# Optimization experiments

Hardware: AMD Instinct MI355X
Metric: run time of the kernel (lower is better)

## Reference

```python
import jax, jax.numpy as jnp
import numpy as np

HEADS = 8
DIM_HEAD = 64
SCALE = DIM_HEAD ** -0.5


def setup_inputs() -> dict:
    key = jax.random.key(0)
    ks = jax.random.split(key, 6)
    b, n, d = 2, 4096, 1024
    inner = HEADS * DIM_HEAD  # 512
    x = jax.random.normal(ks[0], (b, n, d), dtype=jnp.float32)
    Wq = jax.random.normal(ks[1], (d, inner), dtype=jnp.float32) * (d ** -0.5)
    Wk = jax.random.normal(ks[2], (d, inner), dtype=jnp.float32) * (d ** -0.5)
    Wv = jax.random.normal(ks[3], (d, inner), dtype=jnp.float32) * (d ** -0.5)
    Wout = jax.random.normal(ks[4], (inner, d), dtype=jnp.float32) * (inner ** -0.5)
    bout = jnp.zeros((d,), dtype=jnp.float32)
    return {"x": x, "Wq": Wq, "Wk": Wk, "Wv": Wv, "Wout": Wout, "bout": bout}


def reference(x, Wq, Wk, Wv, Wout, bout):
    b, n, _ = x.shape
    h, dh = HEADS, DIM_HEAD
    # self-attention: context = x
    q = (x @ Wq).reshape(b, n, h, dh).transpose(0, 2, 1, 3)  # b h n d
    k = (x @ Wk).reshape(b, n, h, dh).transpose(0, 2, 1, 3)
    v = (x @ Wv).reshape(b, n, h, dh).transpose(0, 2, 1, 3)
    sim = jnp.einsum('bhid,bhjd->bhij', q, k) * SCALE  # full score matrix
    attn = jax.nn.softmax(sim, axis=-1)
    out = jnp.einsum('bhij,bhjd->bhid', attn, v)
    out = out.transpose(0, 2, 1, 3).reshape(b, n, h * dh)  # b n (h d)
    return out @ Wout + bout
```

## Files before the change

### kernel.cpp

```cpp
#include <hip/hip_runtime.h>
#include <hip/hip_bf16.h>

typedef __bf16 bf16x8 __attribute__((ext_vector_type(8)));
typedef __bf16 bf16x4 __attribute__((ext_vector_type(4)));
typedef float floatx4 __attribute__((ext_vector_type(4)));

#define MFMA16(a, b, c) __builtin_amdgcn_mfma_f32_16x16x32_bf16((a), (b), (c), 0, 0, 0)

__device__ __forceinline__ void stage16(const __bf16* g, __bf16* lds_base) {
  __builtin_amdgcn_global_load_lds(
      (__attribute__((address_space(1))) void*)(void*)g,
      (__attribute__((address_space(3))) void*)lds_base, 16, 0, 0);
}

__global__ void detect_dtype(const unsigned int* __restrict__ x, int* __restrict__ flag) {
  __shared__ int cnt;
  if (threadIdx.x == 0) cnt = 0;
  __syncthreads();
  int c = 0;
  for (int i = threadIdx.x; i < 4096; i += 256) {
    const unsigned f = (x[i] >> 7) & 0xFF;
    c += (f >= 100 && f <= 140) ? 1 : 0;
  }
  atomicAdd(&cnt, c);
  __syncthreads();
  if (threadIdx.x == 0) *flag = (cnt > 2048) ? 1 : 0;
}

__global__ __launch_bounds__(256) void transpose3_conv(
    const void* __restrict__ s0, const void* __restrict__ s1,
    const void* __restrict__ s2, __bf16* __restrict__ dst,
    int R, int C, const int* __restrict__ flagp) {
  __shared__ __bf16 t[32][33];
  const int isbf = *flagp;
  const void* src = (blockIdx.z == 0) ? s0 : (blockIdx.z == 1) ? s1 : s2;
  __bf16* d = dst + (size_t)blockIdx.z * R * C;
  const int bx = blockIdx.x * 32, by = blockIdx.y * 32;
  const int x = threadIdx.x & 31, y0 = threadIdx.x >> 5;
#pragma unroll
  for (int i = y0; i < 32; i += 8) {
    const size_t idx = (size_t)(by + i) * C + bx + x;
    t[i][x] = isbf ? ((const __bf16*)src)[idx] : (__bf16)(((const float*)src)[idx]);
  }
  __syncthreads();
#pragma unroll
  for (int i = y0; i < 32; i += 8) d[(size_t)(bx + i) * R + by + x] = t[x][i];
}

__global__ __launch_bounds__(256) void transpose_conv(const void* __restrict__ src,
                                                      __bf16* __restrict__ dst,
                                                      int R, int C,
                                                      const int* __restrict__ flagp) {
  __shared__ __bf16 t[32][33];
  const int isbf = *flagp;
  const int bx = blockIdx.x * 32, by = blockIdx.y * 32;
  const int x = threadIdx.x & 31, y0 = threadIdx.x >> 5;
#pragma unroll
  for (int i = y0; i < 32; i += 8) {
    const size_t idx = (size_t)(by + i) * C + bx + x;
    t[i][x] = isbf ? ((const __bf16*)src)[idx] : (__bf16)(((const float*)src)[idx]);
  }
  __syncthreads();
#pragma unroll
  for (int i = y0; i < 32; i += 8) dst[(size_t)(bx + i) * R + by + x] = t[x][i];
}

__global__ __launch_bounds__(256) void vp_transpose(const __bf16* __restrict__ V,
                                                    __bf16* __restrict__ VP) {
  alignas(16) __shared__ __bf16 t[64][64];
  const int bh = blockIdx.y, s0 = blockIdx.x * 64;
  const int row = threadIdx.x >> 2, part = threadIdx.x & 3;
  const __bf16* src = V + (size_t)bh * 262144 + (size_t)(s0 + row) * 64 + part * 16;
  *(bf16x8*)&t[row][part * 16] = *(const bf16x8*)src;
  *(bf16x8*)&t[row][part * 16 + 8] = *(const bf16x8*)(src + 8);
  __syncthreads();
  const int d = row, og = part;
  bf16x8 w0, w1;
#pragma unroll
  for (int e = 0; e < 8; e++) {
    const int o0 = og * 16 + e, o1 = og * 16 + 8 + e;
    w0[e] = t[(o0 & 3) * 16 + (o0 >> 2)][d];
    w1[e] = t[(o1 & 3) * 16 + (o1 >> 2)][d];
  }
  __bf16* dst = VP + (size_t)bh * 262144 + (size_t)d * 4096 + s0 + og * 16;
  *(bf16x8*)dst = w0;
  *(bf16x8*)(dst + 8) = w1;
}

template <int A_DUAL>
__global__ __launch_bounds__(256) void gemm_bt(
    const void* __restrict__ Araw, const __bf16* __restrict__ Bt,
    void* __restrict__ Cv, void* __restrict__ Cv2, int M, int N, int K,
    const void* __restrict__ bias, int permute, int egress_dual,
    size_t zsB, size_t zsC, const int* __restrict__ flagp) {
  alignas(16) __shared__ __bf16 As[128 * 32];
  alignas(16) __shared__ __bf16 Bs[128 * 32];
  const int isbf = *flagp;
  Bt += blockIdx.z * zsB;
  const size_t zoff = (size_t)blockIdx.z * zsC;
  const int tid = threadIdx.x;
  const int wave = tid >> 6, lane = tid & 63;
  const int m0 = blockIdx.y * 128, n0 = blockIdx.x * 128;
  const int wm = (wave & 1) * 64, wn = (wave >> 1) * 64;
  const int fr = lane & 15, fq = lane >> 4;

  const floatx4 zero4 = {0.f, 0.f, 0.f, 0.f};
  floatx4 acc[4][4];
#pragma unroll
  for (int i = 0; i < 4; i++)
#pragma unroll
    for (int j = 0; j < 4; j++) acc[i][j] = zero4;

  const int lrow = lane >> 2;
  const int lk = (lane & 3) * 8;

  for (int k0 = 0; k0 < K; k0 += 32) {
#pragma unroll
    for (int cc = 0; cc < 2; ++cc) {
      const int c = 2 * wave + cc;
      const size_t aoff = (size_t)(m0 + c * 16 + lrow) * K + k0 + lk;
      if (A_DUAL && !isbf) {
        const float* p = (const float*)Araw + aoff;
        const float4 f0 = *(const float4*)p;
        const float4 f1 = *(const float4*)(p + 4);
        bf16x8 v;
        v[0] = (__bf16)f0.x; v[1] = (__bf16)f0.y; v[2] = (__bf16)f0.z; v[3] = (__bf16)f0.w;
        v[4] = (__bf16)f1.x; v[5] = (__bf16)f1.y; v[6] = (__bf16)f1.z; v[7] = (__bf16)f1.w;
        *(bf16x8*)&As[c * 512 + lane * 8] = v;
      } else {
        stage16((const __bf16*)Araw + aoff, &As[c * 512]);
      }
      stage16(Bt + (size_t)(n0 + c * 16 + lrow) * K + k0 + lk, &Bs[c * 512]);
    }
    __syncthreads();
    bf16x8 af[4], bg[4];
#pragma unroll
    for (int mt = 0; mt < 4; mt++)
      af[mt] = *(const bf16x8*)&As[(wm + mt * 16 + fr) * 32 + fq * 8];
#pragma unroll
    for (int nt = 0; nt < 4; nt++)
      bg[nt] = *(const bf16x8*)&Bs[(wn + nt * 16 + fr) * 32 + fq * 8];
#pragma unroll
    for (int mt = 0; mt < 4; mt++)
#pragma unroll
      for (int nt = 0; nt < 4; nt++)
        acc[mt][nt] = MFMA16(af[mt], bg[nt], acc[mt][nt]);
    __syncthreads();
  }

  const float qs = (permute && blockIdx.z == 0) ? 0.18033688011112042f
                                                : 1.0f;
#pragma unroll
  for (int mt = 0; mt < 4; mt++)
#pragma unroll
    for (int nt = 0; nt < 4; nt++)
#pragma unroll
      for (int r = 0; r < 4; r++) {
        const int row = m0 + wm + mt * 16 + fq * 4 + r;
        const int col = n0 + wn + nt * 16 + fr;
        float v = acc[mt][nt][r] * qs;
        if (bias)
          v += isbf ? (float)((const __bf16*)bias)[col] : ((const float*)bias)[col];
        if (permute) {
          const int bh = (row >> 12) * 8 + (col >> 6);
          const int s = row & 4095, d = col & 63;
          const size_t pidx = (size_t)bh * 262144 + (size_t)s * 64 + d;
          if (blockIdx.z == 2)
            ((__bf16*)Cv2)[pidx] = (__bf16)v;
          else
            ((__bf16*)Cv)[zoff + pidx] = (__bf16)v;
        } else {
          const size_t idx = (size_t)row * N + col;
          if (egress_dual && !isbf)
            ((float*)Cv)[idx] = v;
          else
            ((__bf16*)Cv)[idx] = (__bf16)v;
        }
      }
}

#define ATT_S 4096
#define KV_SPLIT 2
__global__ __launch_bounds__(512, 4) void attn_flash(
    const __bf16* __restrict__ Qa, const __bf16* __restrict__ Ka,
    const __bf16* __restrict__ VPa, float* __restrict__ Of,
    float* __restrict__ lp) {
  alignas(16) __shared__ __bf16 Kl[2][64 * 64];
  alignas(16) __shared__ __bf16 Vl[2][64 * 64];
  alignas(16) __shared__ __bf16 Pl[8 * 32 * 64];
  const int tid = threadIdx.x, wave = tid >> 6, lane = tid & 63;
  const int bh = blockIdx.y, b = bh >> 3, h = bh & 7;
  const int z = blockIdx.z;
  const int q0 = blockIdx.x * 256 + wave * 32;
  const int fr = lane & 15, fq = lane >> 4;
  const __bf16* Qb = Qa + (size_t)bh * ATT_S * 64;
  const __bf16* Kb = Ka + (size_t)bh * ATT_S * 64;
  const __bf16* Vb = VPa + (size_t)bh * ATT_S * 64;

  const int sw0 = ((fq ^ (fr & 7)) * 8);
  const int sw1 = (((fq + 4) ^ (fr & 7)) * 8);
  const int r0 = tid >> 3;
  const int ssw = (((tid & 7) ^ (r0 & 7)) * 8);

  bf16x8 aq[2][2];
#pragma unroll
  for (int mt = 0; mt < 2; mt++)
#pragma unroll
    for (int kt = 0; kt < 2; kt++)
      aq[mt][kt] = *(const bf16x8*)(Qb + (size_t)(q0 + mt * 16 + fr) * 64 + kt * 32 + fq * 8);

  const floatx4 zero4 = {0.f, 0.f, 0.f, 0.f};
  floatx4 o[2][4];
  float lsum[2][4];
#pragma unroll
  for (int mt = 0; mt < 2; mt++) {
#pragma unroll
    for (int nt = 0; nt < 4; nt++) o[mt][nt] = zero4;
#pragma unroll
    for (int r = 0; r < 4; r++) lsum[mt][r] = 0.f;
  }

  const int JT = (ATT_S / 64) / KV_SPLIT;
  const int jbase = z * JT;

  stage16(Kb + (size_t)(jbase * 64 + r0) * 64 + ssw, &Kl[0][wave * 512]);
  stage16(Vb + (size_t)r0 * 4096 + jbase * 64 + ssw, &Vl[0][wave * 512]);

  for (int j = 0; j < JT; ++j) {
    __syncthreads();
    const int cur = j & 1;
    if (j + 1 < JT) {
      const int kv1 = (jbase + j + 1) * 64;
      stage16(Kb + (size_t)(kv1 + r0) * 64 + ssw, &Kl[1 - cur][wave * 512]);
      stage16(Vb + (size_t)r0 * 4096 + kv1 + ssw, &Vl[1 - cur][wave * 512]);
    }
    const __bf16* Klc = Kl[cur];
    const __bf16* Vlc = Vl[cur];

    floatx4 s4[2][4];
    __builtin_amdgcn_s_setprio(1);
#pragma unroll
    for (int nt = 0; nt < 4; nt++) {
      bf16x8 bk0 = *(const bf16x8*)&Klc[(nt * 16 + fr) * 64 + sw0];
      bf16x8 bk1 = *(const bf16x8*)&Klc[(nt * 16 + fr) * 64 + sw1];
#pragma unroll
      for (int mt = 0; mt < 2; mt++) {
        floatx4 zz = zero4;
        zz = MFMA16(aq[mt][0], bk0, zz);
        zz = MFMA16(aq[mt][1], bk1, zz);
        s4[mt][nt] = zz;
      }
    }
    __builtin_amdgcn_s_setprio(0);

#pragma unroll
    for (int mt = 0; mt < 2; mt++)
#pragma unroll
      for (int r = 0; r < 4; r++) {
        bf16x4 pv;
        float psum = 0.f;
#pragma unroll
        for (int nt = 0; nt < 4; nt++) {
          const float p = __builtin_amdgcn_exp2f(s4[mt][nt][r]);
          pv[nt] = (__bf16)p;
          psum += p;
        }
        lsum[mt][r] += psum;
        const int row = wave * 32 + mt * 16 + fq * 4 + r;
        const int vg = (fr >> 1) ^ ((fq * 4 + r) & 7);
        *(bf16x4*)&Pl[row * 64 + vg * 8 + (fr & 1) * 4] = pv;
      }
    asm volatile("s_waitcnt lgkmcnt(0)" ::: "memory");

    bf16x8 bv[4][2];
#pragma unroll
    for (int nt = 0; nt < 4; nt++) {
      bv[nt][0] = *(const bf16x8*)&Vlc[(nt * 16 + fr) * 64 + sw0];
      bv[nt][1] = *(const bf16x8*)&Vlc[(nt * 16 + fr) * 64 + sw1];
    }
    __builtin_amdgcn_s_setprio(1);
#pragma unroll
    for (int mt = 0; mt < 2; mt++) {
      const int prow = (wave * 32 + mt * 16 + fr) * 64;
      bf16x8 ap0 = *(const bf16x8*)&Pl[prow + sw0];
      bf16x8 ap1 = *(const bf16x8*)&Pl[prow + sw1];
#pragma unroll
      for (int nt = 0; nt < 4; nt++) {
        o[mt][nt] = MFMA16(ap0, bv[nt][0], o[mt][nt]);
        o[mt][nt] = MFMA16(ap1, bv[nt][1], o[mt][nt]);
      }
    }
    __builtin_amdgcn_s_setprio(0);
  }

#pragma unroll
  for (int off = 1; off < 16; off <<= 1)
#pragma unroll
    for (int mt = 0; mt < 2; mt++)
#pragma unroll
      for (int r = 0; r < 4; r++) lsum[mt][r] += __shfl_xor(lsum[mt][r], off, 64);

  float* Ofz = Of + (size_t)z * 8192 * 512;
  float* lz = lp + (size_t)z * 16 * 4096;
#pragma unroll
  for (int mt = 0; mt < 2; mt++)
#pragma unroll
    for (int r = 0; r < 4; r++) {
      const int row = q0 + mt * 16 + fq * 4 + r;
      if (fr == 0) lz[bh * 4096 + row] = lsum[mt][r];
#pragma unroll
      for (int nt = 0; nt < 4; nt++) {
        const int col = h * 64 + nt * 16 + fr;
        Ofz[(size_t)(b * ATT_S + row) * 512 + col] = o[mt][nt][r];
      }
    }
}

__global__ __launch_bounds__(256) void attn_combine(
    const float* __restrict__ Of, const float* __restrict__ lp,
    __bf16* __restrict__ O) {
  const size_t i = ((size_t)blockIdx.x * 256 + threadIdx.x) * 8;
  const int row = (int)(i >> 9), colb = (int)(i & 511);
  const int bh = (row >> 12) * 8 + (colb >> 6), qrow = row & 4095;
  const float l = lp[bh * 4096 + qrow] + lp[16 * 4096 + bh * 4096 + qrow];
  const float inv = 1.0f / l;
  const float4 a0 = *(const float4*)(Of + i);
  const float4 a1 = *(const float4*)(Of + i + 4);
  const float4 b0 = *(const float4*)(Of + 8192 * 512 + i);
  const float4 b1 = *(const float4*)(Of + 8192 * 512 + i + 4);
  bf16x8 w;
  w[0] = (__bf16)((a0.x + b0.x) * inv); w[1] = (__bf16)((a0.y + b0.y) * inv);
  w[2] = (__bf16)((a0.z + b0.z) * inv); w[3] = (__bf16)((a0.w + b0.w) * inv);
  w[4] = (__bf16)((a1.x + b1.x) * inv); w[5] = (__bf16)((a1.y + b1.y) * inv);
  w[6] = (__bf16)((a1.z + b1.z) * inv); w[7] = (__bf16)((a1.w + b1.w) * inv);
  *(bf16x8*)(O + i) = w;
}

extern "C" void kernel_launch(void* const* d_in, const int* in_sizes, int n_in,
                              void* d_out, int out_size, void* d_ws, size_t ws_size,
                              hipStream_t stream) {
  (void)in_sizes; (void)n_in; (void)out_size; (void)ws_size;
  const void* x = d_in[0];
  const void* Wq = d_in[1];
  const void* Wk = d_in[2];
  const void* Wv = d_in[3];
  const void* Wout = d_in[4];
  const void* bout = d_in[5];

  char* ws = (char*)d_ws;
  int* flag = (int*)ws;
  __bf16* wtq = (__bf16*)(ws + (1u << 20));
  __bf16* wto = (__bf16*)(ws + (4u << 20));
  __bf16* Q = (__bf16*)(ws + (5u << 20));
  __bf16* K = (__bf16*)(ws + (13u << 20));
  __bf16* VP = (__bf16*)(ws + (21u << 20));
  __bf16* O = (__bf16*)(ws + (29u << 20));
  __bf16* Vtmp = O;
  float* Of = (float*)(ws + (38u << 20));
  float* lp = (float*)(ws + (72u << 20));

  detect_dtype<<<1, 256, 0, stream>>>((const unsigned int*)x, flag);

  transpose3_conv<<<dim3(16, 32, 3), 256, 0, stream>>>(Wq, Wk, Wv, wtq, 1024, 512, flag);
  transpose_conv<<<dim3(32, 16), 256, 0, stream>>>(Wout, wto, 512, 1024, flag);

  gemm_bt<1><<<dim3(4, 64, 3), 256, 0, stream>>>(
      x, wtq, Q, Vtmp, 8192, 512, 1024, nullptr, 1, 0,
      (size_t)512 * 1024, (size_t)8192 * 512, flag);

  vp_transpose<<<dim3(64, 16), 256, 0, stream>>>(Vtmp, VP);

  attn_flash<<<dim3(ATT_S / 256, 16, KV_SPLIT), 512, 0, stream>>>(Q, K, VP, Of, lp);

  attn_combine<<<2048, 256, 0, stream>>>(Of, lp, O);

  gemm_bt<0><<<dim3(8, 64, 1), 256, 0, stream>>>(
      O, wto, d_out, nullptr, 8192, 1024, 512, bout, 0, 1, 0, 0, flag);
}
```

Baseline: 282.1 us.

## Use 4 waves with 64 query rows each in flash attention

The attention kernel now runs 256 threads (4 waves) per block instead of 512. Each wave handles 64 query rows instead of 32, and the K/V staging loads are doubled per thread to cover the tile. This raises the reuse of the K and V LDS fragments per wave, since they are loaded once per tile and used across four M-tiles, and it halves the number of waves contending at the barrier. In exchange it uses more registers for the accumulators and Q fragments, and there are fewer waves per block to hide latency.

Measured after the change: 285.7 us. No clear change (+1.3%).

```diff
diff --git a/kernel.cpp b/kernel.cpp
--- a/kernel.cpp
+++ b/kernel.cpp
@@ -181,17 +181,17 @@
 
 #define ATT_S 4096
 #define KV_SPLIT 2
-__global__ __launch_bounds__(512, 4) void attn_flash(
+__global__ __launch_bounds__(256, 2) void attn_flash(
     const __bf16* __restrict__ Qa, const __bf16* __restrict__ Ka,
     const __bf16* __restrict__ VPa, float* __restrict__ Of,
     float* __restrict__ lp) {
   alignas(16) __shared__ __bf16 Kl[2][64 * 64];
   alignas(16) __shared__ __bf16 Vl[2][64 * 64];
-  alignas(16) __shared__ __bf16 Pl[8 * 32 * 64];
+  alignas(16) __shared__ __bf16 Pl[4 * 64 * 64];
   const int tid = threadIdx.x, wave = tid >> 6, lane = tid & 63;
   const int bh = blockIdx.y, b = bh >> 3, h = bh & 7;
   const int z = blockIdx.z;
-  const int q0 = blockIdx.x * 256 + wave * 32;
+  const int q0 = blockIdx.x * 256 + wave * 64;
   const int fr = lane & 15, fq = lane >> 4;
   const __bf16* Qb = Qa + (size_t)bh * ATT_S * 64;
   const __bf16* Kb = Ka + (size_t)bh * ATT_S * 64;
@@ -202,18 +202,18 @@
   const int r0 = tid >> 3;
   const int ssw = (((tid & 7) ^ (r0 & 7)) * 8);
 
-  bf16x8 aq[2][2];
-#pragma unroll
-  for (int mt = 0; mt < 2; mt++)
+  bf16x8 aq[4][2];
+#pragma unroll
+  for (int mt = 0; mt < 4; mt++)
 #pragma unroll
     for (int kt = 0; kt < 2; kt++)
       aq[mt][kt] = *(const bf16x8*)(Qb + (size_t)(q0 + mt * 16 + fr) * 64 + kt * 32 + fq * 8);
 
   const floatx4 zero4 = {0.f, 0.f, 0.f, 0.f};
-  floatx4 o[2][4];
-  float lsum[2][4];
-#pragma unroll
-  for (int mt = 0; mt < 2; mt++) {
+  floatx4 o[4][4];
+  float lsum[4][4];
+#pragma unroll
+  for (int mt = 0; mt < 4; mt++) {
 #pragma unroll
     for (int nt = 0; nt < 4; nt++) o[mt][nt] = zero4;
 #pragma unroll
@@ -224,7 +224,9 @@
   const int jbase = z * JT;
 
   stage16(Kb + (size_t)(jbase * 64 + r0) * 64 + ssw, &Kl[0][wave * 512]);
+  stage16(Kb + (size_t)(jbase * 64 + 32 + r0) * 64 + ssw, &Kl[0][2048 + wave * 512]);
   stage16(Vb + (size_t)r0 * 4096 + jbase * 64 + ssw, &Vl[0][wave * 512]);
+  stage16(Vb + (size_t)(32 + r0) * 4096 + jbase * 64 + ssw, &Vl[0][2048 + wave * 512]);
 
   for (int j = 0; j < JT; ++j) {
     __syncthreads();
@@ -232,78 +234,83 @@
     if (j + 1 < JT) {
       const int kv1 = (jbase + j + 1) * 64;
       stage16(Kb + (size_t)(kv1 + r0) * 64 + ssw, &Kl[1 - cur][wave * 512]);
+      stage16(Kb + (size_t)(kv1 + 32 + r0) * 64 + ssw, &Kl[1 - cur][2048 + wave * 512]);
       stage16(Vb + (size_t)r0 * 4096 + kv1 + ssw, &Vl[1 - cur][wave * 512]);
+      stage16(Vb + (size_t)(32 + r0) * 4096 + kv1 + ssw, &Vl[1 - cur][2048 + wave * 512]);
     }
     const __bf16* Klc = Kl[cur];
     const __bf16* Vlc = Vl[cur];
 
-    floatx4 s4[2][4];
-    __builtin_amdgcn_s_setprio(1);
+    bf16x8 fk[4][2];
 #pragma unroll
     for (int nt = 0; nt < 4; nt++) {
-      bf16x8 bk0 = *(const bf16x8*)&Klc[(nt * 16 + fr) * 64 + sw0];
-      bf16x8 bk1 = *(const bf16x8*)&Klc[(nt * 16 + fr) * 64 + sw1];
-#pragma unroll
-      for (int mt = 0; mt < 2; mt++) {
+      fk[nt][0] = *(const bf16x8*)&Klc[(nt * 16 + fr) * 64 + sw0];
+      fk[nt][1] = *(const bf16x8*)&Klc[(nt * 16 + fr) * 64 + sw1];
+    }
+
+#pragma unroll
+    for (int mt = 0; mt < 4; mt++) {
+      floatx4 s4[4];
+      __builtin_amdgcn_s_setprio(1);
+#pragma unroll
+      for (int nt = 0; nt < 4; nt++) {
         floatx4 zz = zero4;
-        zz = MFMA16(aq[mt][0], bk0, zz);
-        zz = MFMA16(aq[mt][1], bk1, zz);
-        s4[mt][nt] = zz;
-      }
-    }
-    __builtin_amdgcn_s_setprio(0);
-
-#pragma unroll
-    for (int mt = 0; mt < 2; mt++)
+        zz = MFMA16(aq[mt][0], fk[nt][0], zz);
+        zz = MFMA16(aq[mt][1], fk[nt][1], zz);
+        s4[nt] = zz;
+      }
+      __builtin_amdgcn_s_setprio(0);
 #pragma unroll
       for (int r = 0; r < 4; r++) {
         bf16x4 pv;
         float psum = 0.f;
 #pragma unroll
         for (int nt = 0; nt < 4; nt++) {
-          const float p = __builtin_amdgcn_exp2f(s4[mt][nt][r]);
+          const float p = __builtin_amdgcn_exp2f(s4[nt][r]);
           pv[nt] = (__bf16)p;
           psum += p;
         }
         lsum[mt][r] += psum;
-        const int row = wave * 32 + mt * 16 + fq * 4 + r;
+        const int row = wave * 64 + mt * 16 + fq * 4 + r;
         const int vg = (fr >> 1) ^ ((fq * 4 + r) & 7);
         *(bf16x4*)&Pl[row * 64 + vg * 8 + (fr & 1) * 4] = pv;
       }
+    }
+
+    bf16x8 fv[4][2];
+#pragma unroll
+    for (int nt = 0; nt < 4; nt++) {
+      fv[nt][0] = *(const bf16x8*)&Vlc[(nt * 16 + fr) * 64 + sw0];
+      fv[nt][1] = *(const bf16x8*)&Vlc[(nt * 16 + fr) * 64 + sw1];
+    }
     asm volatile("s_waitcnt lgkmcnt(0)" ::: "memory");
 
-    bf16x8 bv[4][2];
-#pragma unroll
-    for (int nt = 0; nt < 4; nt++) {
-      bv[nt][0] = *(const bf16x8*)&Vlc[(nt * 16 + fr) * 64 + sw0];
-      bv[nt][1] = *(const bf16x8*)&Vlc[(nt * 16 + fr) * 64 + sw1];
-    }
-    __builtin_amdgcn_s_setprio(1);
-#pragma unroll
-    for (int mt = 0; mt < 2; mt++) {
-      const int prow = (wave * 32 + mt * 16 + fr) * 64;
+#pragma unroll
+    for (int mt = 0; mt < 4; mt++) {
+      const int prow = (wave * 64 + mt * 16 + fr) * 64;
       bf16x8 ap0 = *(const bf16x8*)&Pl[prow + sw0];
       bf16x8 ap1 = *(const bf16x8*)&Pl[prow + sw1];
+      __builtin_amdgcn_s_setprio(1);
 #pragma unroll
       for (int nt = 0; nt < 4; nt++) {
-        o[mt][nt] = MFMA16(ap0, bv[nt][0], o[mt][nt]);
-        o[mt][nt] = MFMA16(ap1, bv[nt][1], o[mt][nt]);
-      }
-    }
-    __builtin_amdgcn_s_setprio(0);
+        o[mt][nt] = MFMA16(ap0, fv[nt][0], o[mt][nt]);
+        o[mt][nt] = MFMA16(ap1, fv[nt][1], o[mt][nt]);
+      }
+      __builtin_amdgcn_s_setprio(0);
+    }
   }
 
 #pragma unroll
   for (int off = 1; off < 16; off <<= 1)
 #pragma unroll
-    for (int mt = 0; mt < 2; mt++)
+    for (int mt = 0; mt < 4; mt++)
 #pragma unroll
       for (int r = 0; r < 4; r++) lsum[mt][r] += __shfl_xor(lsum[mt][r], off, 64);
 
   float* Ofz = Of + (size_t)z * 8192 * 512;
   float* lz = lp + (size_t)z * 16 * 4096;
 #pragma unroll
-  for (int mt = 0; mt < 2; mt++)
+  for (int mt = 0; mt < 4; mt++)
 #pragma unroll
     for (int r = 0; r < 4; r++) {
       const int row = q0 + mt * 16 + fq * 4 + r;
@@ -370,7 +377,7 @@
 
   vp_transpose<<<dim3(64, 16), 256, 0, stream>>>(Vtmp, VP);
 
-  attn_flash<<<dim3(ATT_S / 256, 16, KV_SPLIT), 512, 0, stream>>>(Q, K, VP, Of, lp);
+  attn_flash<<<dim3(ATT_S / 256, 16, KV_SPLIT), 256, 0, stream>>>(Q, K, VP, Of, lp);
 
   attn_combine<<<2048, 256, 0, stream>>>(Of, lp, O);
 
```
